# Performance work log

Hardware: AMD Instinct MI355X
Metric: run time of the kernel (lower is better)

## Reference

```python
import jax, jax.numpy as jnp
import numpy as np

EMBED_DIM = 1024
NHEAD = 16
HEAD_DIM = EMBED_DIM // NHEAD  # 64
B, S = 2, 2048


def _rotate_half(x):
    x1, x2 = jnp.split(x, 2, axis=-1)
    return jnp.concatenate([-x2, x1], axis=-1)


def _apply_rope(t, cos, sin):
    # t: (B, H, S, Dh); cos/sin: (S, Dh) broadcast over leading dims
    return t * cos + _rotate_half(t) * sin


def setup_inputs() -> dict:
    key = jax.random.key(0)
    ks = jax.random.split(key, 6)
    x = jax.random.normal(ks[0], (B, S, EMBED_DIM), dtype=jnp.float32)
    # real RoPE tables: theta_i = 10000^(-2i/Dh), duplicated for the two halves
    inv_freq = 1.0 / (10000.0 ** (jnp.arange(0, HEAD_DIM, 2, dtype=jnp.float32) / HEAD_DIM))
    freqs = jnp.outer(jnp.arange(S, dtype=jnp.float32), inv_freq)  # (S, Dh/2)
    emb = jnp.concatenate([freqs, freqs], axis=-1)  # (S, Dh)
    cos = jnp.cos(emb)
    sin = jnp.sin(emb)
    W_in = jax.random.normal(ks[1], (EMBED_DIM, 3 * EMBED_DIM), dtype=jnp.float32) * 0.02
    b_in = jax.random.normal(ks[2], (3 * EMBED_DIM,), dtype=jnp.float32) * 0.02
    W_out = jax.random.normal(ks[3], (EMBED_DIM, EMBED_DIM), dtype=jnp.float32) * 0.02
    b_out = jax.random.normal(ks[4], (EMBED_DIM,), dtype=jnp.float32) * 0.02
    return {"x": x, "cos": cos, "sin": sin, "W_in": W_in, "b_in": b_in,
            "W_out": W_out, "b_out": b_out}


def reference(x, cos, sin, W_in, b_in, W_out, b_out):
    Bs, Ss, D = x.shape
    qkv = x @ W_in + b_in  # (B, S, 3D)
    q, k, v = jnp.split(qkv, 3, axis=-1)
    # (B, S, D) -> (B, H, S, Dh)
    def heads(t):
        return t.reshape(Bs, Ss, NHEAD, HEAD_DIM).transpose(0, 2, 1, 3)
    q, k, v = heads(q), heads(k), heads(v)
    q = _apply_rope(q, cos, sin)
    k = _apply_rope(k, cos, sin)
    scale = 1.0 / jnp.sqrt(jnp.array(HEAD_DIM, dtype=x.dtype))
    scores = jnp.einsum('bhqd,bhkd->bhqk', q, k) * scale
    attn = jax.nn.softmax(scores, axis=-1)
    out = jnp.einsum('bhqk,bhkd->bhqd', attn, v)
    out = out.transpose(0, 2, 1, 3).reshape(Bs, Ss, D)
    return out @ W_out + b_out
```

## Files before the change

kernel.cpp:

```cpp
#include <hip/hip_runtime.h>
#include <hip/hip_bf16.h>

typedef float f32x4 __attribute__((ext_vector_type(4)));
typedef short s16x8 __attribute__((ext_vector_type(8)));

typedef const __attribute__((address_space(1))) unsigned int* as1u;
typedef __attribute__((address_space(3))) unsigned int* as3u;

__device__ __forceinline__ unsigned short f2bf(float f) {
    union { float f; unsigned u; } v; v.f = f;
    unsigned u = v.u;
    u += 0x7fffu + ((u >> 16) & 1u);
    return (unsigned short)(u >> 16);
}

__device__ __forceinline__ void gload16(const void* g, void* l3) {
    __builtin_amdgcn_global_load_lds((as1u)g, (as3u)l3, 16, 0, 0);
}

__device__ __forceinline__ int swzo(int row, int cb) {
    return row * 128 + (cb ^ ((row & 7) << 4));
}

#define LOG2E 1.4426950408889634f
#define QSCALE (0.125f * LOG2E)

__global__ __launch_bounds__(256) void prep_kernel(
    const float* __restrict__ x, unsigned short* __restrict__ xb,
    const float* __restrict__ W_in, unsigned short* __restrict__ Wt_in,
    const float* __restrict__ W_out, unsigned short* __restrict__ Wot)
{
    const int t = threadIdx.x;
    int blk = blockIdx.x;
    if (blk < 2048) {
        size_t i = ((size_t)blk * 256 + t) * 8;
        float4 a = *(const float4*)&x[i];
        float4 b = *(const float4*)&x[i + 4];
        s16x8 p;
        p[0] = (short)f2bf(a.x); p[1] = (short)f2bf(a.y);
        p[2] = (short)f2bf(a.z); p[3] = (short)f2bf(a.w);
        p[4] = (short)f2bf(b.x); p[5] = (short)f2bf(b.y);
        p[6] = (short)f2bf(b.z); p[7] = (short)f2bf(b.w);
        *(s16x8*)&xb[i] = p;
        return;
    }
    const float* W;
    unsigned short* Wt;
    int N;
    if (blk < 2816) { blk -= 2048; W = W_in;  Wt = Wt_in; N = 3072; }
    else            { blk -= 2816; W = W_out; Wt = Wot;   N = 1024; }
    __shared__ alignas(16) short T[64 * 64];
    const int KB = 16;
    const int kb = blk % KB, nb = blk / KB;
#pragma unroll
    for (int pass = 0; pass < 4; ++pass) {
        int k = pass * 16 + (t >> 4);
        int n4 = (t & 15) * 4;
        float4 v = *(const float4*)&W[(size_t)(kb * 64 + k) * N + nb * 64 + n4];
        short4 s4;
        s4.x = (short)f2bf(v.x); s4.y = (short)f2bf(v.y);
        s4.z = (short)f2bf(v.z); s4.w = (short)f2bf(v.w);
        *(short4*)((char*)T + k * 128 + ((n4 * 2) ^ ((k & 7) << 4))) = s4;
    }
    __syncthreads();
#pragma unroll
    for (int pass = 0; pass < 4; ++pass) {
        int n = pass * 16 + (t >> 4);
        int k4 = (t & 15) * 4;
        short4 s4;
        s4.x = *(const short*)((const char*)T + (k4 + 0) * 128 + ((n * 2) ^ (((k4 + 0) & 7) << 4)));
        s4.y = *(const short*)((const char*)T + (k4 + 1) * 128 + ((n * 2) ^ (((k4 + 1) & 7) << 4)));
        s4.z = *(const short*)((const char*)T + (k4 + 2) * 128 + ((n * 2) ^ (((k4 + 2) & 7) << 4)));
        s4.w = *(const short*)((const char*)T + (k4 + 3) * 128 + ((n * 2) ^ (((k4 + 3) & 7) << 4)));
        *(short4*)&Wt[(size_t)(nb * 64 + n) * 1024 + kb * 64 + k4] = s4;
    }
}

__global__ __launch_bounds__(256) void qkv_rope_kernel(
    const unsigned short* __restrict__ xb, const unsigned short* __restrict__ Wt,
    const float* __restrict__ bias, const float* __restrict__ cosb,
    const float* __restrict__ sinb,
    unsigned short* __restrict__ Qb, unsigned short* __restrict__ Kb,
    unsigned short* __restrict__ Vb)
{
    __shared__ alignas(16) short As[128 * 64];
    __shared__ alignas(16) short Bs[128 * 64];
    const int bid = blockIdx.x;
    const int mb = bid & 31, nb = bid >> 5;
    const int t = threadIdx.x, w = t >> 6, l = t & 63;
    const int g = l >> 4, j = l & 15;
    const int wm = w >> 1, wn = w & 1;
    const int m0 = mb * 128, n0 = nb * 128;

    f32x4 acc[4][4];
#pragma unroll
    for (int mi = 0; mi < 4; ++mi)
#pragma unroll
        for (int ni = 0; ni < 4; ++ni) acc[mi][ni] = (f32x4){0.f, 0.f, 0.f, 0.f};

    for (int kt = 0; kt < 1024; kt += 64) {
#pragma unroll
        for (int i = 0; i < 4; ++i) {
            int pos = (w * 4 + i) * 1024 + l * 16;
            int r = pos >> 7;
            int lb = (pos & 127) ^ ((r & 7) << 4);
            gload16(&Wt[(size_t)(n0 + r) * 1024 + kt + (lb >> 1)],
                    (char*)Bs + (w * 4 + i) * 1024);
            gload16(&xb[(size_t)(m0 + r) * 1024 + kt + (lb >> 1)],
                    (char*)As + (w * 4 + i) * 1024);
        }
        __syncthreads();
#pragma unroll
        for (int kf = 0; kf < 2; ++kf) {
            s16x8 af[4], bv[4];
#pragma unroll
            for (int mi = 0; mi < 4; ++mi)
                af[mi] = *(const s16x8*)((const char*)As + swzo(wm * 64 + mi * 16 + j, kf * 64 + g * 16));
#pragma unroll
            for (int ni = 0; ni < 4; ++ni)
                bv[ni] = *(const s16x8*)((const char*)Bs + swzo(wn * 64 + ni * 16 + j, kf * 64 + g * 16));
#pragma unroll
            for (int mi = 0; mi < 4; ++mi)
#pragma unroll
                for (int ni = 0; ni < 4; ++ni)
                    acc[mi][ni] = __builtin_amdgcn_mfma_f32_16x16x32_bf16(af[mi], bv[ni], acc[mi][ni], 0, 0, 0);
        }
        __syncthreads();
    }

    const int row0 = m0 + wm * 64;
    const int col0 = n0 + wn * 64;
    const int sec = col0 >> 10;
    const int h = (col0 & 1023) >> 6;

    if (sec < 2) {
        unsigned short* dst = (sec == 0) ? Qb : Kb;
        const float qs = (sec == 0) ? QSCALE : 1.0f;
#pragma unroll
        for (int nt = 0; nt < 2; ++nt) {
            const int d = nt * 16 + j;
            const float b1 = bias[col0 + d];
            const float b2 = bias[col0 + d + 32];
#pragma unroll
            for (int mi = 0; mi < 4; ++mi) {
#pragma unroll
                for (int r = 0; r < 4; ++r) {
                    int row = row0 + mi * 16 + g * 4 + r;
                    int s = row & 2047, bb = row >> 11;
                    float c = cosb[s * 64 + d], sn = sinb[s * 64 + d];
                    float x1 = acc[mi][nt][r] + b1;
                    float x2 = acc[mi][nt + 2][r] + b2;
                    float lo = (x1 * c - x2 * sn) * qs;
                    float hi = (x1 * sn + x2 * c) * qs;
                    size_t base = ((size_t)(bb * 16 + h) * 2048 + s) * 64;
                    dst[base + d] = f2bf(lo);
                    dst[base + d + 32] = f2bf(hi);
                }
            }
        }
    } else {
#pragma unroll
        for (int nt = 0; nt < 4; ++nt) {
            const int d = nt * 16 + j;
            const float bvv = bias[col0 + d];
#pragma unroll
            for (int mi = 0; mi < 4; ++mi) {
#pragma unroll
                for (int r = 0; r < 4; ++r) {
                    int row = row0 + mi * 16 + g * 4 + r;
                    int s = row & 2047, bb = row >> 11;
                    size_t base = ((size_t)(bb * 16 + h) * 2048 + s) * 64;
                    Vb[base + d] = f2bf(acc[mi][nt][r] + bvv);
                }
            }
        }
    }
}

#define NROUND 16
__global__ __launch_bounds__(512, 4) void attn_kernel(
    const unsigned short* __restrict__ Qb, const unsigned short* __restrict__ Kb,
    const unsigned short* __restrict__ Vb, unsigned short* __restrict__ AO)
{
    __shared__ alignas(16) short Ks[2][2 * 64 * 64];
    __shared__ alignas(16) short Vt[2][2 * 64 * 64];
    const int bid = blockIdx.x;
    const int bh = (bid & 7) + ((bid >> 7) << 3);
    const int qt = (bid >> 3) & 15;
    const int t = threadIdx.x, w = t >> 6, l = t & 63;
    const int g = l >> 4, j = l & 15;
    const unsigned short* Qh = Qb + (size_t)bh * 131072;
    const unsigned short* Kh = Kb + (size_t)bh * 131072;
    const unsigned short* Vh = Vb + (size_t)bh * 131072;
    const int q0 = qt * 128 + w * 16;

    s16x8 aq[2];
    aq[0] = *(const s16x8*)&Qh[(size_t)(q0 + j) * 64 + g * 8];
    aq[1] = *(const s16x8*)&Qh[(size_t)(q0 + j) * 64 + 32 + g * 8];

    float lt_ = 0.f;
    f32x4 o[4];
#pragma unroll
    for (int dt = 0; dt < 4; ++dt) o[dt] = (f32x4){0.f, 0.f, 0.f, 0.f};

    const bool vrole = (w < 4);
    const int tv = t & 255;
    const int vk = (tv & 31) * 2;
    const int vd = (tv >> 5) * 8;
    const int kw = (w & 3);

    s16x8 va[2], vb2[2];

    if (vrole) {
#pragma unroll
        for (int s = 0; s < 2; ++s) {
            va[s]  = *(const s16x8*)&Vh[(size_t)(s * 64 + vk) * 64 + vd];
            vb2[s] = *(const s16x8*)&Vh[(size_t)(s * 64 + vk + 1) * 64 + vd];
        }
    } else {
#pragma unroll
        for (int i = 0; i < 4; ++i) {
            int p = (kw * 4 + i) * 1024 + l * 16;
            int s = p >> 13, q = p & 8191;
            int r = q >> 7, lb = (q & 127) ^ ((r & 7) << 4);
            gload16(&Kh[(size_t)(s * 64 + r) * 64 + (lb >> 1)],
                    (char*)Ks[0] + (kw * 4 + i) * 1024);
        }
    }
    asm volatile("s_waitcnt vmcnt(0)" ::: "memory");
    if (vrole) {
#pragma unroll
        for (int s = 0; s < 2; ++s)
#pragma unroll
            for (int dd = 0; dd < 8; ++dd) {
                int d = vd + dd;
                unsigned pkv = (unsigned)(unsigned short)va[s][dd] | ((unsigned)(unsigned short)vb2[s][dd] << 16);
                *(unsigned*)((char*)Vt[0] + s * 8192 + d * 128 + ((vk * 2) ^ ((d & 7) << 4))) = pkv;
            }
    }
    asm volatile("s_waitcnt lgkmcnt(0)" ::: "memory");
    __builtin_amdgcn_s_barrier();

    for (int rr = 0; rr < NROUND; ++rr) {
        const int cur = rr & 1, nxt = cur ^ 1;
        const int kvp = ((rr + 1) & (NROUND - 1)) * 128;

        if (vrole) {
#pragma unroll
            for (int s = 0; s < 2; ++s) {
                va[s]  = *(const s16x8*)&Vh[(size_t)(kvp + s * 64 + vk) * 64 + vd];
                vb2[s] = *(const s16x8*)&Vh[(size_t)(kvp + s * 64 + vk + 1) * 64 + vd];
            }
        } else {
#pragma unroll
            for (int i = 0; i < 4; ++i) {
                int p = (kw * 4 + i) * 1024 + l * 16;
                int s = p >> 13, q = p & 8191;
                int r = q >> 7, lb = (q & 127) ^ ((r & 7) << 4);
                gload16(&Kh[(size_t)(kvp + s * 64 + r) * 64 + (lb >> 1)],
                        (char*)Ks[nxt] + (kw * 4 + i) * 1024);
            }
        }

        f32x4 sc[2][4];
#pragma unroll
        for (int sub = 0; sub < 2; ++sub)
#pragma unroll
            for (int nt = 0; nt < 4; ++nt) sc[sub][nt] = (f32x4){0.f, 0.f, 0.f, 0.f};
        __builtin_amdgcn_s_setprio(1);
#pragma unroll
        for (int sub = 0; sub < 2; ++sub) {
            const char* kbase = (const char*)Ks[cur] + sub * 8192;
#pragma unroll
            for (int kf = 0; kf < 2; ++kf) {
                s16x8 bk[4];
#pragma unroll
                for (int nt = 0; nt < 4; ++nt)
                    bk[nt] = *(const s16x8*)(kbase + swzo(nt * 16 + j, kf * 64 + g * 16));
#pragma unroll
                for (int nt = 0; nt < 4; ++nt)
                    sc[sub][nt] = __builtin_amdgcn_mfma_f32_16x16x32_bf16(bk[nt], aq[kf], sc[sub][nt], 0, 0, 0);
            }
        }
        __builtin_amdgcn_s_setprio(0);

#pragma unroll
        for (int sub = 0; sub < 2; ++sub) {
            const char* vbase = (const char*)Vt[cur] + sub * 8192;

            float rs = 0.f;
#pragma unroll
            for (int nt = 0; nt < 4; ++nt)
#pragma unroll
                for (int r = 0; r < 4; ++r) {
                    sc[sub][nt][r] = __builtin_amdgcn_exp2f(sc[sub][nt][r]);
                    rs += sc[sub][nt][r];
                }
            lt_ += rs;

            unsigned pk[4][2];
#pragma unroll
            for (int nt = 0; nt < 4; ++nt)
#pragma unroll
                for (int s = 0; s < 2; ++s)
                    asm("v_cvt_pk_bf16_f32 %0, %1, %2"
                        : "=v"(pk[nt][s]) : "v"(sc[sub][nt][2 * s]), "v"(sc[sub][nt][2 * s + 1]));

#pragma unroll
            for (int kf = 0; kf < 2; ++kf) {
                unsigned A0 = pk[2 * kf][0], A1 = pk[2 * kf][1];
                unsigned B0 = pk[2 * kf + 1][0], B1 = pk[2 * kf + 1][1];
                asm("v_permlane32_swap_b32 %0, %1" : "+v"(A0), "+v"(B0));
                asm("v_permlane32_swap_b32 %0, %1" : "+v"(A1), "+v"(B1));
                asm("v_permlane16_swap_b32 %0, %1" : "+v"(A0), "+v"(B0));
                asm("v_permlane16_swap_b32 %0, %1" : "+v"(A1), "+v"(B1));
                union { unsigned u[4]; s16x8 v; } fr;
                fr.u[0] = A0;
                fr.u[1] = A1;
                fr.u[2] = B0;
                fr.u[3] = B1;
                __builtin_amdgcn_s_setprio(1);
#pragma unroll
                for (int dt = 0; dt < 4; ++dt) {
                    s16x8 vb = *(const s16x8*)(vbase + swzo(dt * 16 + j, kf * 64 + g * 16));
                    o[dt] = __builtin_amdgcn_mfma_f32_16x16x32_bf16(fr.v, vb, o[dt], 0, 0, 0);
                }
                __builtin_amdgcn_s_setprio(0);
            }
        }

        if (vrole) {
#pragma unroll
            for (int s = 0; s < 2; ++s)
#pragma unroll
                for (int dd = 0; dd < 8; ++dd) {
                    int d = vd + dd;
                    unsigned pkv = (unsigned)(unsigned short)va[s][dd] | ((unsigned)(unsigned short)vb2[s][dd] << 16);
                    *(unsigned*)((char*)Vt[nxt] + s * 8192 + d * 128 + ((vk * 2) ^ ((d & 7) << 4))) = pkv;
                }
        }
        asm volatile("s_waitcnt vmcnt(0) lgkmcnt(0)" ::: "memory");
        __builtin_amdgcn_s_barrier();
    }

    lt_ += __shfl_xor(lt_, 16);
    lt_ += __shfl_xor(lt_, 32);

    const int b = bh >> 4, h = bh & 15;
#pragma unroll
    for (int r = 0; r < 4; ++r) {
        float inv = 1.0f / __shfl(lt_, g * 4 + r);
        int s = q0 + g * 4 + r;
        size_t base = ((size_t)b * 2048 + s) * 1024 + h * 64;
#pragma unroll
        for (int dt = 0; dt < 4; ++dt)
            AO[base + dt * 16 + j] = f2bf(o[dt][r] * inv);
    }
}

__global__ __launch_bounds__(256) void out_gemm_kernel(
    const unsigned short* __restrict__ A, const unsigned short* __restrict__ Wot,
    const float* __restrict__ bias, float* __restrict__ out)
{
    __shared__ alignas(16) short As[128 * 64];
    __shared__ alignas(16) short Bs[128 * 64];
    const int bid = blockIdx.x;
    const int mb = bid & 31, nb = bid >> 5;
    const int t = threadIdx.x, w = t >> 6, l = t & 63;
    const int g = l >> 4, j = l & 15;
    const int wm = w >> 1, wn = w & 1;
    const int m0 = mb * 128, n0 = nb * 128;

    f32x4 acc[4][4];
#pragma unroll
    for (int mi = 0; mi < 4; ++mi)
#pragma unroll
        for (int ni = 0; ni < 4; ++ni) acc[mi][ni] = (f32x4){0.f, 0.f, 0.f, 0.f};

    for (int kt = 0; kt < 1024; kt += 64) {
#pragma unroll
        for (int i = 0; i < 4; ++i) {
            int pos = (w * 4 + i) * 1024 + l * 16;
            int r = pos >> 7;
            int lb = (pos & 127) ^ ((r & 7) << 4);
            gload16(&A[(size_t)(m0 + r) * 1024 + kt + (lb >> 1)],
                    (char*)As + (w * 4 + i) * 1024);
            gload16(&Wot[(size_t)(n0 + r) * 1024 + kt + (lb >> 1)],
                    (char*)Bs + (w * 4 + i) * 1024);
        }
        __syncthreads();
#pragma unroll
        for (int kf = 0; kf < 2; ++kf) {
            s16x8 af[4], bv[4];
#pragma unroll
            for (int mi = 0; mi < 4; ++mi)
                af[mi] = *(const s16x8*)((const char*)As + swzo(wm * 64 + mi * 16 + j, kf * 64 + g * 16));
#pragma unroll
            for (int ni = 0; ni < 4; ++ni)
                bv[ni] = *(const s16x8*)((const char*)Bs + swzo(wn * 64 + ni * 16 + j, kf * 64 + g * 16));
#pragma unroll
            for (int mi = 0; mi < 4; ++mi)
#pragma unroll
                for (int ni = 0; ni < 4; ++ni)
                    acc[mi][ni] = __builtin_amdgcn_mfma_f32_16x16x32_bf16(af[mi], bv[ni], acc[mi][ni], 0, 0, 0);
        }
        __syncthreads();
    }

    const int row0 = m0 + wm * 64;
    const int col0 = n0 + wn * 64;
#pragma unroll
    for (int ni = 0; ni < 4; ++ni) {
        const int col = col0 + ni * 16 + j;
        const float bvv = bias[col];
#pragma unroll
        for (int mi = 0; mi < 4; ++mi)
#pragma unroll
            for (int r = 0; r < 4; ++r) {
                int row = row0 + mi * 16 + g * 4 + r;
                out[(size_t)row * 1024 + col] = acc[mi][ni][r] + bvv;
            }
    }
}

extern "C" void kernel_launch(void* const* d_in, const int* in_sizes, int n_in,
                              void* d_out, int out_size, void* d_ws, size_t ws_size,
                              hipStream_t stream) {
    const float* x     = (const float*)d_in[0];
    const float* cosb  = (const float*)d_in[1];
    const float* sinb  = (const float*)d_in[2];
    const float* W_in  = (const float*)d_in[3];
    const float* b_in  = (const float*)d_in[4];
    const float* W_out = (const float*)d_in[5];
    const float* b_out = (const float*)d_in[6];
    float* out = (float*)d_out;

    const size_t HBUF = 2ull * 16 * 2048 * 64;
    if (ws_size < (4 * HBUF + 1024 * 1024) * sizeof(unsigned short)) return;
    unsigned short* Qb = (unsigned short*)d_ws;
    unsigned short* Kb = Qb + HBUF;
    unsigned short* Vb = Kb + HBUF;
    unsigned short* R  = Vb + HBUF;
    unsigned short* Wt_in = R;
    unsigned short* AO    = R;
    unsigned short* Wot   = R + HBUF;
    unsigned short* xbuf  = (unsigned short*)d_out;

    hipLaunchKernelGGL(prep_kernel, dim3(3072), dim3(256), 0, stream,
                       x, xbuf, W_in, Wt_in, W_out, Wot);
    hipLaunchKernelGGL(qkv_rope_kernel, dim3(768), dim3(256), 0, stream,
                       xbuf, Wt_in, b_in, cosb, sinb, Qb, Kb, Vb);
    hipLaunchKernelGGL(attn_kernel, dim3(512), dim3(512), 0, stream,
                       Qb, Kb, Vb, AO);
    hipLaunchKernelGGL(out_gemm_kernel, dim3(256), dim3(256), 0, stream,
                       AO, Wot, b_out, out);
}
```

Measured before the change: 122.5 us.

## Split attention key blocks across wave pairs, each wave owning two query tiles

Each pair of waves now shares 32 query rows, and each wave in the pair handles half of every 64-key sub-block. Every K and V fragment read from LDS then feeds two MFMAs (one per query tile) instead of one, which halves LDS read traffic per MFMA. The two partial outputs and row sums are combined at the end through shared memory with an extra __syncthreads. The cost is more registers (two accumulator sets and Q fragments) and a reduction epilogue.

New measurement: 128.3 us. 4.7% more time.

```diff
diff --git a/kernel.cpp b/kernel.cpp
--- a/kernel.cpp
+++ b/kernel.cpp
@@ -189,19 +189,25 @@
     const int qt = (bid >> 3) & 15;
     const int t = threadIdx.x, w = t >> 6, l = t & 63;
     const int g = l >> 4, j = l & 15;
+    const int pr = w >> 1, hf = w & 1;
     const unsigned short* Qh = Qb + (size_t)bh * 131072;
     const unsigned short* Kh = Kb + (size_t)bh * 131072;
     const unsigned short* Vh = Vb + (size_t)bh * 131072;
-    const int q0 = qt * 128 + w * 16;
-
-    s16x8 aq[2];
-    aq[0] = *(const s16x8*)&Qh[(size_t)(q0 + j) * 64 + g * 8];
-    aq[1] = *(const s16x8*)&Qh[(size_t)(q0 + j) * 64 + 32 + g * 8];
-
-    float lt_ = 0.f;
-    f32x4 o[4];
-#pragma unroll
-    for (int dt = 0; dt < 4; ++dt) o[dt] = (f32x4){0.f, 0.f, 0.f, 0.f};
+    const int q0 = qt * 128 + pr * 32;
+
+    s16x8 aq[2][2];
+#pragma unroll
+    for (int m = 0; m < 2; ++m)
+#pragma unroll
+        for (int kf = 0; kf < 2; ++kf)
+            aq[m][kf] = *(const s16x8*)&Qh[(size_t)(q0 + m * 16 + j) * 64 + kf * 32 + g * 8];
+
+    float lt0 = 0.f, lt1 = 0.f;
+    f32x4 o[2][4];
+#pragma unroll
+    for (int m = 0; m < 2; ++m)
+#pragma unroll
+        for (int dt = 0; dt < 4; ++dt) o[m][dt] = (f32x4){0.f, 0.f, 0.f, 0.f};
 
     const bool vrole = (w < 4);
     const int tv = t & 255;
@@ -262,71 +268,74 @@
             }
         }
 
-        f32x4 sc[2][4];
-#pragma unroll
-        for (int sub = 0; sub < 2; ++sub)
-#pragma unroll
-            for (int nt = 0; nt < 4; ++nt) sc[sub][nt] = (f32x4){0.f, 0.f, 0.f, 0.f};
-        __builtin_amdgcn_s_setprio(1);
 #pragma unroll
         for (int sub = 0; sub < 2; ++sub) {
             const char* kbase = (const char*)Ks[cur] + sub * 8192;
+            const char* vbase = (const char*)Vt[cur] + sub * 8192;
+
+            f32x4 sc[2][2];
+#pragma unroll
+            for (int m = 0; m < 2; ++m)
+#pragma unroll
+                for (int nt = 0; nt < 2; ++nt) sc[m][nt] = (f32x4){0.f, 0.f, 0.f, 0.f};
+            __builtin_amdgcn_s_setprio(1);
 #pragma unroll
             for (int kf = 0; kf < 2; ++kf) {
-                s16x8 bk[4];
-#pragma unroll
-                for (int nt = 0; nt < 4; ++nt)
-                    bk[nt] = *(const s16x8*)(kbase + swzo(nt * 16 + j, kf * 64 + g * 16));
-#pragma unroll
-                for (int nt = 0; nt < 4; ++nt)
-                    sc[sub][nt] = __builtin_amdgcn_mfma_f32_16x16x32_bf16(bk[nt], aq[kf], sc[sub][nt], 0, 0, 0);
-            }
-        }
-        __builtin_amdgcn_s_setprio(0);
-
-#pragma unroll
-        for (int sub = 0; sub < 2; ++sub) {
-            const char* vbase = (const char*)Vt[cur] + sub * 8192;
-
-            float rs = 0.f;
-#pragma unroll
-            for (int nt = 0; nt < 4; ++nt)
+                s16x8 bk[2];
+#pragma unroll
+                for (int nt = 0; nt < 2; ++nt)
+                    bk[nt] = *(const s16x8*)(kbase + swzo(hf * 32 + nt * 16 + j, kf * 64 + g * 16));
+#pragma unroll
+                for (int m = 0; m < 2; ++m)
+#pragma unroll
+                    for (int nt = 0; nt < 2; ++nt)
+                        sc[m][nt] = __builtin_amdgcn_mfma_f32_16x16x32_bf16(bk[nt], aq[m][kf], sc[m][nt], 0, 0, 0);
+            }
+            __builtin_amdgcn_s_setprio(0);
+
+            float rs0 = 0.f, rs1 = 0.f;
+#pragma unroll
+            for (int nt = 0; nt < 2; ++nt)
 #pragma unroll
                 for (int r = 0; r < 4; ++r) {
-                    sc[sub][nt][r] = __builtin_amdgcn_exp2f(sc[sub][nt][r]);
-                    rs += sc[sub][nt][r];
+                    sc[0][nt][r] = __builtin_amdgcn_exp2f(sc[0][nt][r]);
+                    rs0 += sc[0][nt][r];
+                    sc[1][nt][r] = __builtin_amdgcn_exp2f(sc[1][nt][r]);
+                    rs1 += sc[1][nt][r];
                 }
-            lt_ += rs;
-
-            unsigned pk[4][2];
-#pragma unroll
-            for (int nt = 0; nt < 4; ++nt)
-#pragma unroll
-                for (int s = 0; s < 2; ++s)
-                    asm("v_cvt_pk_bf16_f32 %0, %1, %2"
-                        : "=v"(pk[nt][s]) : "v"(sc[sub][nt][2 * s]), "v"(sc[sub][nt][2 * s + 1]));
-
-#pragma unroll
-            for (int kf = 0; kf < 2; ++kf) {
-                unsigned A0 = pk[2 * kf][0], A1 = pk[2 * kf][1];
-                unsigned B0 = pk[2 * kf + 1][0], B1 = pk[2 * kf + 1][1];
+            lt0 += rs0; lt1 += rs1;
+
+            unsigned pk[2][2][2];
+#pragma unroll
+            for (int m = 0; m < 2; ++m)
+#pragma unroll
+                for (int nt = 0; nt < 2; ++nt)
+#pragma unroll
+                    for (int s = 0; s < 2; ++s)
+                        asm("v_cvt_pk_bf16_f32 %0, %1, %2"
+                            : "=v"(pk[m][nt][s]) : "v"(sc[m][nt][2 * s]), "v"(sc[m][nt][2 * s + 1]));
+
+            union { unsigned u[4]; s16x8 v; } fr[2];
+#pragma unroll
+            for (int m = 0; m < 2; ++m) {
+                unsigned A0 = pk[m][0][0], A1 = pk[m][0][1];
+                unsigned B0 = pk[m][1][0], B1 = pk[m][1][1];
                 asm("v_permlane32_swap_b32 %0, %1" : "+v"(A0), "+v"(B0));
                 asm("v_permlane32_swap_b32 %0, %1" : "+v"(A1), "+v"(B1));
                 asm("v_permlane16_swap_b32 %0, %1" : "+v"(A0), "+v"(B0));
                 asm("v_permlane16_swap_b32 %0, %1" : "+v"(A1), "+v"(B1));
-                union { unsigned u[4]; s16x8 v; } fr;
-                fr.u[0] = A0;
-                fr.u[1] = A1;
-                fr.u[2] = B0;
-                fr.u[3] = B1;
-                __builtin_amdgcn_s_setprio(1);
-#pragma unroll
-                for (int dt = 0; dt < 4; ++dt) {
-                    s16x8 vb = *(const s16x8*)(vbase + swzo(dt * 16 + j, kf * 64 + g * 16));
-                    o[dt] = __builtin_amdgcn_mfma_f32_16x16x32_bf16(fr.v, vb, o[dt], 0, 0, 0);
-                }
-                __builtin_amdgcn_s_setprio(0);
-            }
+                fr[m].u[0] = A0; fr[m].u[1] = A1; fr[m].u[2] = B0; fr[m].u[3] = B1;
+            }
+
+            __builtin_amdgcn_s_setprio(1);
+#pragma unroll
+            for (int dt = 0; dt < 4; ++dt) {
+                s16x8 vb = *(const s16x8*)(vbase + swzo(dt * 16 + j, hf * 64 + g * 16));
+#pragma unroll
+                for (int m = 0; m < 2; ++m)
+                    o[m][dt] = __builtin_amdgcn_mfma_f32_16x16x32_bf16(fr[m].v, vb, o[m][dt], 0, 0, 0);
+            }
+            __builtin_amdgcn_s_setprio(0);
         }
 
         if (vrole) {
@@ -343,18 +352,50 @@
         __builtin_amdgcn_s_barrier();
     }
 
-    lt_ += __shfl_xor(lt_, 16);
-    lt_ += __shfl_xor(lt_, 32);
-
-    const int b = bh >> 4, h = bh & 15;
-#pragma unroll
-    for (int r = 0; r < 4; ++r) {
-        float inv = 1.0f / __shfl(lt_, g * 4 + r);
-        int s = q0 + g * 4 + r;
-        size_t base = ((size_t)b * 2048 + s) * 1024 + h * 64;
-#pragma unroll
-        for (int dt = 0; dt < 4; ++dt)
-            AO[base + dt * 16 + j] = f2bf(o[dt][r] * inv);
+    lt0 += __shfl_xor(lt0, 16); lt0 += __shfl_xor(lt0, 32);
+    lt1 += __shfl_xor(lt1, 16); lt1 += __shfl_xor(lt1, 32);
+
+    float* obuf  = (float*)Ks;
+    float* ltbuf = (float*)Vt;
+    if (hf == 1) {
+#pragma unroll
+        for (int m = 0; m < 2; ++m)
+#pragma unroll
+            for (int dt = 0; dt < 4; ++dt)
+#pragma unroll
+                for (int r = 0; r < 4; ++r)
+                    obuf[pr * 2048 + m * 1024 + dt * 256 + (g * 4 + r) * 16 + j] = o[m][dt][r];
+        if (l < 16) {
+            ltbuf[pr * 32 + j] = lt0;
+            ltbuf[pr * 32 + 16 + j] = lt1;
+        }
+    }
+    __syncthreads();
+    if (hf == 0) {
+#pragma unroll
+        for (int m = 0; m < 2; ++m)
+#pragma unroll
+            for (int dt = 0; dt < 4; ++dt)
+#pragma unroll
+                for (int r = 0; r < 4; ++r)
+                    o[m][dt][r] += obuf[pr * 2048 + m * 1024 + dt * 256 + (g * 4 + r) * 16 + j];
+        lt0 += ltbuf[pr * 32 + j];
+        lt1 += ltbuf[pr * 32 + 16 + j];
+
+        const int b = bh >> 4, h = bh & 15;
+#pragma unroll
+        for (int m = 0; m < 2; ++m) {
+            float ltm = m ? lt1 : lt0;
+#pragma unroll
+            for (int r = 0; r < 4; ++r) {
+                float inv = 1.0f / __shfl(ltm, g * 4 + r);
+                int s = q0 + m * 16 + g * 4 + r;
+                size_t base = ((size_t)b * 2048 + s) * 1024 + h * 64;
+#pragma unroll
+                for (int dt = 0; dt < 4; ++dt)
+                    AO[base + dt * 16 + j] = f2bf(o[m][dt][r] * inv);
+            }
+        }
     }
 }
 
```
